# Kernel tuning notes

Measured on AMD Instinct MI355X. Metric: run time of the kernel, lower is better.

## Reference

```python
import jax, jax.numpy as jnp
import numpy as np

B, S, D, H = 2, 2048, 1024, 16
HEAD_DIM = D // H
THETA = 10000.0


def setup_inputs() -> dict:
    key = jax.random.key(0)
    kx, kq, kk, kv, ko = jax.random.split(key, 5)
    w_scale = jnp.float32(D ** -0.5)  # keep logits O(1)
    return {
        "x": jax.random.normal(kx, (B, S, D), dtype=jnp.float32),
        "WQ": jax.random.normal(kq, (D, D), dtype=jnp.float32) * w_scale,
        "WK": jax.random.normal(kk, (D, D), dtype=jnp.float32) * w_scale,
        "WV": jax.random.normal(kv, (D, D), dtype=jnp.float32) * w_scale,
        "WO": jax.random.normal(ko, (D, D), dtype=jnp.float32) * w_scale,
        "token_positions": jnp.arange(S, dtype=jnp.int32),
    }


def _rope(x, pos, theta):
    # x: [B, H, S, dh]; pos: [S]. Interleaved (even, odd) pair rotation.
    dh = x.shape[-1]
    inv_freq = theta ** (-jnp.arange(0, dh, 2, dtype=jnp.float32) / dh)  # [dh/2]
    ang = pos.astype(jnp.float32)[:, None] * inv_freq                    # [S, dh/2]
    cos, sin = jnp.cos(ang), jnp.sin(ang)
    x1, x2 = x[..., 0::2], x[..., 1::2]
    r1 = x1 * cos - x2 * sin
    r2 = x1 * sin + x2 * cos
    return jnp.stack([r1, r2], axis=-1).reshape(x.shape)


def reference(x, WQ, WK, WV, WO, token_positions):
    Bs, Ss, Dm = x.shape
    dh = Dm // H
    # QKV projections (Linear with no bias, y = x @ W.T), split heads -> [B,H,S,dh]
    q = (x @ WQ.T).reshape(Bs, Ss, H, dh).transpose(0, 2, 1, 3)
    k = (x @ WK.T).reshape(Bs, Ss, H, dh).transpose(0, 2, 1, 3)
    v = (x @ WV.T).reshape(Bs, Ss, H, dh).transpose(0, 2, 1, 3)
    q = _rope(q, token_positions, THETA)
    k = _rope(k, token_positions, THETA)
    scores = jnp.einsum("bhqd,bhkd->bhqk", q, k) * jnp.float32(dh ** -0.5)
    causal = jnp.tril(jnp.ones((Ss, Ss), dtype=bool))
    scores = jnp.where(causal, scores, jnp.finfo(scores.dtype).min)
    attn = jax.nn.softmax(scores, axis=-1)
    out = jnp.einsum("bhqk,bhkd->bhqd", attn, v)
    out = out.transpose(0, 2, 1, 3).reshape(Bs, Ss, Dm)
    return out @ WO.T
```

## Files before the change

kernel.cpp:

```cpp
#include <hip/hip_runtime.h>
#include <hip/hip_bf16.h>


#define S_LEN 2048
#define NHEADS 16
#define NEG_SENT -30000.0f

typedef __attribute__((ext_vector_type(8))) short short8;
typedef __attribute__((ext_vector_type(4))) float f32x4;
typedef unsigned int u32;
typedef unsigned short u16;

static __device__ __forceinline__ float bf2f(u16 u) {
  union { u32 i; float f; } v; v.i = ((u32)u) << 16; return v.f;
}
static __device__ __forceinline__ u16 f2bf(float f) {
  union { float f; u32 i; } v; v.f = f;
  u32 u = v.i;
  u32 r = (u + 0x7fffu + ((u >> 16) & 1u)) >> 16;
  return (u16)r;
}
static __device__ __forceinline__ u32 cvtpk(float a, float b) {
  u32 r;
  asm("v_cvt_pk_bf16_f32 %0, %1, %2" : "=v"(r) : "v"(a), "v"(b));
  return r;
}

static __device__ __forceinline__ void glds16(const void* g, void* l) {
  __builtin_amdgcn_global_load_lds((const __attribute__((address_space(1))) u32*)g,
                                   (__attribute__((address_space(3))) u32*)l, 16, 0, 0);
}

__global__ void convert_kernel(const float* __restrict__ x, const float* __restrict__ wq,
                               const float* __restrict__ wk, const float* __restrict__ wv,
                               const float* __restrict__ wo, u16* __restrict__ xb,
                               u16* __restrict__ wb) {
  int i = blockIdx.x * blockDim.x + threadIdx.x;
  const float* src; u16* dst; int off;
  if (i < 1048576) { src = x; dst = xb; off = i; }
  else {
    int j = i - 1048576;
    int widx = j >> 18;
    off = j & 262143;
    src = (widx == 0) ? wq : (widx == 1) ? wk : (widx == 2) ? wv : wo;
    dst = wb + (size_t)widx * 1048576;
  }
  float4 v = ((const float4*)src)[off];
  ushort4 o;
  o.x = f2bf(v.x); o.y = f2bf(v.y); o.z = f2bf(v.z); o.w = f2bf(v.w);
  ((ushort4*)dst)[off] = o;
}

__global__ void rope_kernel(u32* __restrict__ Qb, u32* __restrict__ Kb,
                            const int* __restrict__ pos) {
  int i = blockIdx.x * blockDim.x + threadIdx.x;
  int c = i & 511;
  int rowi = i >> 9;
  int s = rowi & (S_LEN - 1);
  int ip = c & 31;
  float p = (float)pos[s];
  float ang = p * __builtin_exp2f((float)ip * -0.41524101186f);
  float sn, cs;
  sincosf(ang, &sn, &cs);
  u32 v = Qb[i];
  float x1 = bf2f((u16)(v & 0xffff)), x2 = bf2f((u16)(v >> 16));
  float r1 = x1 * cs - x2 * sn, r2 = x1 * sn + x2 * cs;
  Qb[i] = (u32)f2bf(r1) | ((u32)f2bf(r2) << 16);
  v = Kb[i];
  x1 = bf2f((u16)(v & 0xffff)); x2 = bf2f((u16)(v >> 16));
  r1 = x1 * cs - x2 * sn; r2 = x1 * sn + x2 * cs;
  Kb[i] = (u32)f2bf(r1) | ((u32)f2bf(r2) << 16);
}

__global__ void vtrans_kernel(const u16* __restrict__ V, u16* __restrict__ Vt) {
  __shared__ u16 T[64][72];
  const int i = blockIdx.x;
  const int st = i & 31;
  const int bh = i >> 5;
  const int tid = threadIdx.x;
  const int r = tid >> 3, c8 = tid & 7;
  const int s0 = st << 6;
  const int b = bh >> 4, h = bh & 15;
  const u16* src = V + (((size_t)(b * S_LEN + s0 + r)) << 10) + (h << 6) + (c8 << 3);
  uint4 v0 = *(const uint4*)src;
  uint4 v1 = *(const uint4*)(src + (32 << 10));
  *(uint4*)&T[r][c8 << 3] = v0;
  *(uint4*)&T[r + 32][c8 << 3] = v1;
  __syncthreads();
#pragma unroll
  for (int hf = 0; hf < 2; hf++) {
    int d = r + (hf << 5);
    ushort4 o1, o2;
    int sl = c8 << 3;
    o1.x = T[sl + 0][d]; o1.y = T[sl + 1][d]; o1.z = T[sl + 2][d]; o1.w = T[sl + 3][d];
    o2.x = T[sl + 4][d]; o2.y = T[sl + 5][d]; o2.z = T[sl + 6][d]; o2.w = T[sl + 7][d];
    u16* dst = Vt + (((size_t)((bh << 6) + d)) << 11) + s0 + sl;
    *(ushort4*)dst = o1;
    *(ushort4*)(dst + 4) = o2;
  }
}

template <int OUTMODE>
__global__ __launch_bounds__(256, 2) void gemm_bt(const u16* __restrict__ A,
                                                  const u16* __restrict__ B,
                                                  u16* __restrict__ o0, u16* __restrict__ o1,
                                                  u16* __restrict__ o2, float* __restrict__ oF,
                                                  int K) {
  __shared__ u16 As[128 * 64];
  __shared__ u16 Bs[128 * 64];
  const int tid = threadIdx.x, w = tid >> 6, l = tid & 63, l15 = l & 15, l4 = l >> 4;
  const int wr = w >> 1, wc = w & 1;
  const int m0 = blockIdx.y << 7, n0 = blockIdx.x << 7;
  const int r = tid >> 3;
  const int swcol = ((tid & 7) << 4) ^ ((r & 7) << 4);
  const char* Ag = (const char*)A + (((size_t)(m0 + r) * K) << 1) + swcol;
  const char* Bg = (const char*)B + (((size_t)(n0 + r) * K) << 1) + swcol;
  char* AsW = (char*)As + (w << 10);
  char* BsW = (char*)Bs + (w << 10);
  const size_t rowskip = ((size_t)32 * K) << 1;
  f32x4 acc[4][4] = {};
  for (int k0 = 0; k0 < K; k0 += 64) {
    __syncthreads();
    const size_t kb = (size_t)k0 << 1;
#pragma unroll
    for (int i = 0; i < 4; i++) {
      glds16(Ag + kb + (size_t)i * rowskip, AsW + i * 4096);
      glds16(Bg + kb + (size_t)i * rowskip, BsW + i * 4096);
    }
    __syncthreads();
#pragma unroll
    for (int kk = 0; kk < 2; kk++) {
      short8 a[4], b[4];
#pragma unroll
      for (int m = 0; m < 4; m++) {
        int row = (wr << 6) + (m << 4) + l15;
        a[m] = *(const short8*)((const char*)As + row * 128 +
                                (((kk << 6) + (l4 << 4)) ^ ((row & 7) << 4)));
      }
#pragma unroll
      for (int n = 0; n < 4; n++) {
        int row = (wc << 6) + (n << 4) + l15;
        b[n] = *(const short8*)((const char*)Bs + row * 128 +
                                (((kk << 6) + (l4 << 4)) ^ ((row & 7) << 4)));
      }
#pragma unroll
      for (int m = 0; m < 4; m++)
#pragma unroll
        for (int n = 0; n < 4; n++)
          acc[m][n] = __builtin_amdgcn_mfma_f32_16x16x32_bf16(a[m], b[n], acc[m][n], 0, 0, 0);
    }
  }
#pragma unroll
  for (int m = 0; m < 4; m++) {
    int grow_b = m0 + (wr << 6) + (m << 4) + (l4 << 2);
#pragma unroll
    for (int n = 0; n < 4; n++) {
      int gcol = n0 + (wc << 6) + (n << 4) + l15;
#pragma unroll
      for (int j = 0; j < 4; j++) {
        int grow = grow_b + j;
        float v = acc[m][n][j];
        if (OUTMODE == 0) {
          u16* base = (gcol < 1024) ? o0 : ((gcol < 2048) ? o1 : o2);
          base[((size_t)grow << 10) + (gcol & 1023)] = f2bf(v);
        } else {
          oF[((size_t)grow << 10) + gcol] = v;
        }
      }
    }
  }
}

__global__ __launch_bounds__(512, 1) void attn_kernel(const u16* __restrict__ Q,
                                                      const u16* __restrict__ K,
                                                      const u16* __restrict__ Vt,
                                                      u16* __restrict__ O) {
  extern __shared__ __align__(16) char smem[];
  const int tid = threadIdx.x, w = tid >> 6, l = tid & 63, l15 = l & 15, g = l >> 4;
  const int grp = w >> 2, w4 = w & 3;
  const int i = blockIdx.x;
  const int xcd = i & 7, slot = i >> 3;
  const int bh = ((slot >> 3) << 3) | xcd;
  const int p = slot & 7;
  const int b = bh >> 4, h = bh & 15;
  const float C2 = 0.125f * 1.44269504089f;
  const int swz = (l15 & 7) << 4;

  const int gt = tid & 255;
  const int r = gt >> 3;
  const int swc = ((gt & 7) << 4) ^ ((r & 7) << 4);
  const char* Kg = (const char*)K + ((size_t)(b * S_LEN + r) << 11) + (h << 7) + swc;
  const char* Vg = (const char*)Vt + ((size_t)((bh << 6) + r) << 12) + swc;
  char* const KsG = smem + (grp << 15);
  char* const VsG = smem + (grp << 15) + 16384;
  char* const Pw = smem + 65536 + (w << 11);
  float* const oMrg = (float*)smem;
  float* const mlMrg = (float*)(smem + 65536);

#define STAGE(T, BSEL)                                              \
  do {                                                              \
    char* kd = KsG + ((BSEL) << 13) + (w4 << 10);                   \
    char* vd = VsG + ((BSEL) << 13) + (w4 << 10);                   \
    const char* ks = Kg + ((size_t)(T) << 17);                      \
    const char* vs = Vg + ((T) << 7);                               \
    glds16(ks, kd);                                                 \
    glds16(ks + (32 << 11), kd + 4096);                             \
    glds16(vs, vd);                                                 \
    glds16(vs + ((size_t)32 << 12), vd + 4096);                     \
  } while (0)

  auto run_qt = [&](int qt) {
    const int q0 = qt << 7;
    const int nr = qt + 1;

    short8 aQ[2][2];
    {
      const int qrow0 = q0 + (w4 << 5) + l15;
      const u16* qp = Q + (((size_t)(b * S_LEN + qrow0)) << 10) + (h << 6) + (g << 3);
      aQ[0][0] = *(const short8*)qp;
      aQ[0][1] = *(const short8*)(qp + 32);
      aQ[1][0] = *(const short8*)(qp + (16 << 10));
      aQ[1][1] = *(const short8*)(qp + (16 << 10) + 32);
    }
    f32x4 o[2][4] = {};
    float m_r[2] = {NEG_SENT, NEG_SENT}, l_r[2] = {0.f, 0.f};

    STAGE(grp, 0);
    __syncthreads();

    for (int rr = 0; rr < nr; ++rr) {
      const int bsel = rr & 1;
      if (rr + 1 < nr) STAGE(2 * (rr + 1) + grp, bsel ^ 1);
      const char* Kbuf = KsG + (bsel << 13);
      const char* Vbuf = VsG + (bsel << 13);
      const int t = 2 * rr + grp;
      const bool domask = (rr == nr - 1);

      f32x4 s[2][4] = {};
#pragma unroll
      for (int kk = 0; kk < 2; ++kk) {
        short8 aK[4];
#pragma unroll
        for (int n = 0; n < 4; ++n) {
          int row = (n << 4) + l15;
          aK[n] = *(const short8*)(Kbuf + row * 128 + (((kk << 6) + (g << 4)) ^ swz));
        }
        __builtin_amdgcn_s_setprio(1);
#pragma unroll
        for (int n = 0; n < 4; ++n) {
          s[0][n] = __builtin_amdgcn_mfma_f32_16x16x32_bf16(aK[n], aQ[0][kk], s[0][n], 0, 0, 0);
          s[1][n] = __builtin_amdgcn_mfma_f32_16x16x32_bf16(aK[n], aQ[1][kk], s[1][n], 0, 0, 0);
        }
        __builtin_amdgcn_s_setprio(0);
      }
      if (domask) {
#pragma unroll
        for (int qs = 0; qs < 2; ++qs) {
          int qg = q0 + (w4 << 5) + (qs << 4) + l15;
#pragma unroll
          for (int n = 0; n < 4; ++n)
#pragma unroll
            for (int jj = 0; jj < 4; ++jj) {
              int key = (t << 6) + (n << 4) + (g << 2) + jj;
              if (key > qg) s[qs][n][jj] = NEG_SENT;
            }
        }
      }
      float mx2[2];
#pragma unroll
      for (int qs = 0; qs < 2; ++qs) {
        float mx = s[qs][0][0];
#pragma unroll
        for (int n = 0; n < 4; ++n)
#pragma unroll
          for (int jj = 0; jj < 4; ++jj) mx = fmaxf(mx, s[qs][n][jj]);
        mx = fmaxf(mx, __shfl_xor(mx, 16));
        mx = fmaxf(mx, __shfl_xor(mx, 32));
        mx2[qs] = mx;
      }
      if (!__all((mx2[0] - m_r[0] <= 44.f) & (mx2[1] - m_r[1] <= 44.f))) {
        float fac[2];
#pragma unroll
        for (int qs = 0; qs < 2; ++qs) {
          float mn = fmaxf(m_r[qs], mx2[qs]);
          float fc = __builtin_exp2f((m_r[qs] - mn) * C2);
          m_r[qs] = mn;
          l_r[qs] *= fc;
          fac[qs] = fc;
        }
#pragma unroll
        for (int qs = 0; qs < 2; ++qs)
#pragma unroll
          for (int jj = 0; jj < 4; ++jj) {
            float fo = __shfl(fac[qs], (g << 2) + jj, 16);
#pragma unroll
            for (int nd = 0; nd < 4; ++nd) o[qs][nd][jj] *= fo;
          }
      }
      short8 aP[2][2];
#pragma unroll
      for (int qs = 0; qs < 2; ++qs) {
        float mC = m_r[qs] * C2;
        float rs = 0.f;
        u32 pk[8];
#pragma unroll
        for (int n = 0; n < 4; ++n) {
          float p0 = __builtin_exp2f(s[qs][n][0] * C2 - mC);
          float p1 = __builtin_exp2f(s[qs][n][1] * C2 - mC);
          float p2 = __builtin_exp2f(s[qs][n][2] * C2 - mC);
          float p3 = __builtin_exp2f(s[qs][n][3] * C2 - mC);
          rs += (p0 + p1) + (p2 + p3);
          pk[2 * n] = cvtpk(p0, p1);
          pk[2 * n + 1] = cvtpk(p2, p3);
        }
        rs += __shfl_xor(rs, 16);
        rs += __shfl_xor(rs, 32);
        l_r[qs] += rs;
        char* pr = Pw + l15 * 128;
#pragma unroll
        for (int n = 0; n < 4; ++n) {
          uint2 pv;
          pv.x = pk[2 * n];
          pv.y = pk[2 * n + 1];
          *(uint2*)(pr + (((n << 5) + (g << 3)) ^ swz)) = pv;
        }
#pragma unroll
        for (int kk = 0; kk < 2; ++kk)
          aP[qs][kk] = *(const short8*)(Pw + l15 * 128 + ((((kk << 6) + (g << 4))) ^ swz));
      }
#pragma unroll
      for (int kk = 0; kk < 2; ++kk) {
        int co = (kk << 6) + (g << 4);
        __builtin_amdgcn_s_setprio(1);
#pragma unroll
        for (int nd = 0; nd < 4; ++nd) {
          int row = (nd << 4) + l15;
          short8 bV = *(const short8*)(Vbuf + row * 128 + (co ^ swz));
          o[0][nd] = __builtin_amdgcn_mfma_f32_16x16x32_bf16(aP[0][kk], bV, o[0][nd], 0, 0, 0);
          o[1][nd] = __builtin_amdgcn_mfma_f32_16x16x32_bf16(aP[1][kk], bV, o[1][nd], 0, 0, 0);
        }
        __builtin_amdgcn_s_setprio(0);
      }
      __syncthreads();
    }

    if (grp == 1) {
      float* ob = oMrg + (w4 << 11);
#pragma unroll
      for (int qs = 0; qs < 2; ++qs)
#pragma unroll
        for (int nd = 0; nd < 4; ++nd)
          *(f32x4*)(ob + (((qs << 2) | nd) << 8) + (l << 2)) = o[qs][nd];
      float* mb = mlMrg + (w4 << 8);
      mb[l] = m_r[0];
      mb[64 + l] = m_r[1];
      mb[128 + l] = l_r[0];
      mb[192 + l] = l_r[1];
    }
    __syncthreads();
    if (grp == 0) {
      float* ob = oMrg + (w4 << 11);
      float* mb = mlMrg + (w4 << 8);
#pragma unroll
      for (int qs = 0; qs < 2; ++qs) {
        float mB = mb[(qs << 6) + l];
        float lB = mb[128 + (qs << 6) + l];
        float mS = fmaxf(m_r[qs], mB);
        float fA = __builtin_exp2f((m_r[qs] - mS) * C2);
        float fB = __builtin_exp2f((mB - mS) * C2);
        float linv = 1.f / (l_r[qs] * fA + lB * fB);
        float sA = fA * linv, sB = fB * linv;
        f32x4 oB[4];
#pragma unroll
        for (int nd = 0; nd < 4; ++nd)
          oB[nd] = *(const f32x4*)(ob + (((qs << 2) | nd) << 8) + (l << 2));
#pragma unroll
        for (int jj = 0; jj < 4; ++jj) {
          float sAo = __shfl(sA, (g << 2) + jj, 16);
          float sBo = __shfl(sB, (g << 2) + jj, 16);
          int qg = q0 + (w4 << 5) + (qs << 4) + (g << 2) + jj;
          u16* orow = O + (((size_t)(b * S_LEN + qg)) << 10) + (h << 6) + l15;
#pragma unroll
          for (int nd = 0; nd < 4; ++nd)
            orow[nd << 4] = f2bf(o[qs][nd][jj] * sAo + oB[nd][jj] * sBo);
        }
      }
    }
    __syncthreads();
  };

  run_qt(p);
  run_qt(15 - p);
#undef STAGE
}

extern "C" void kernel_launch(void* const* d_in, const int* in_sizes, int n_in,
                              void* d_out, int out_size, void* d_ws, size_t ws_size,
                              hipStream_t stream) {
  (void)in_sizes; (void)n_in; (void)out_size; (void)ws_size;
  const float* x = (const float*)d_in[0];
  const float* wq = (const float*)d_in[1];
  const float* wk = (const float*)d_in[2];
  const float* wv = (const float*)d_in[3];
  const float* wo = (const float*)d_in[4];
  const int* pos = (const int*)d_in[5];
  char* ws = (char*)d_ws;
  u16* xb = (u16*)ws;
  u16* wb = (u16*)(ws + ((size_t)8 << 20));
  u16* Qb = (u16*)(ws + ((size_t)16 << 20));
  u16* Kb = (u16*)(ws + ((size_t)24 << 20));
  u16* Vb = (u16*)(ws + ((size_t)32 << 20));
  u16* Ab = (u16*)(ws + ((size_t)40 << 20));
  u16* Vtg = xb;
  float* out = (float*)d_out;

  convert_kernel<<<8192, 256, 0, stream>>>(x, wq, wk, wv, wo, xb, wb);
  dim3 g1(24, 32);
  gemm_bt<0><<<g1, 256, 0, stream>>>(xb, wb, Qb, Kb, Vb, nullptr, 1024);
  rope_kernel<<<8192, 256, 0, stream>>>((u32*)Qb, (u32*)Kb, pos);
  vtrans_kernel<<<1024, 256, 0, stream>>>(Vb, Vtg);
  attn_kernel<<<256, 512, 81920, stream>>>(Qb, Kb, Vtg, Ab);
  dim3 g3(8, 32);
  gemm_bt<1><<<g3, 256, 0, stream>>>(Ab, wb + (size_t)3 * 1048576, nullptr, nullptr, nullptr, out, 1024);
}
```

Baseline: 118.7 us.

## Fuse RoPE and V transpose into QKV GEMM epilogue

Removes the separate rope and V-transpose kernels. RoPE is now applied inside the QKV GEMM epilogue, using a lane shuffle to fetch each value's pair partner, and V is written straight into transposed layout with 4-element vector stores. This saves two kernel launches and several full read/write passes over Q, K and V. In exchange the epilogue does sincos per output element and writes V in a strided pattern.

```diff
diff --git a/kernel.cpp b/kernel.cpp
--- a/kernel.cpp
+++ b/kernel.cpp
@@ -51,61 +51,12 @@
   ((ushort4*)dst)[off] = o;
 }
 
-__global__ void rope_kernel(u32* __restrict__ Qb, u32* __restrict__ Kb,
-                            const int* __restrict__ pos) {
-  int i = blockIdx.x * blockDim.x + threadIdx.x;
-  int c = i & 511;
-  int rowi = i >> 9;
-  int s = rowi & (S_LEN - 1);
-  int ip = c & 31;
-  float p = (float)pos[s];
-  float ang = p * __builtin_exp2f((float)ip * -0.41524101186f);
-  float sn, cs;
-  sincosf(ang, &sn, &cs);
-  u32 v = Qb[i];
-  float x1 = bf2f((u16)(v & 0xffff)), x2 = bf2f((u16)(v >> 16));
-  float r1 = x1 * cs - x2 * sn, r2 = x1 * sn + x2 * cs;
-  Qb[i] = (u32)f2bf(r1) | ((u32)f2bf(r2) << 16);
-  v = Kb[i];
-  x1 = bf2f((u16)(v & 0xffff)); x2 = bf2f((u16)(v >> 16));
-  r1 = x1 * cs - x2 * sn; r2 = x1 * sn + x2 * cs;
-  Kb[i] = (u32)f2bf(r1) | ((u32)f2bf(r2) << 16);
-}
-
-__global__ void vtrans_kernel(const u16* __restrict__ V, u16* __restrict__ Vt) {
-  __shared__ u16 T[64][72];
-  const int i = blockIdx.x;
-  const int st = i & 31;
-  const int bh = i >> 5;
-  const int tid = threadIdx.x;
-  const int r = tid >> 3, c8 = tid & 7;
-  const int s0 = st << 6;
-  const int b = bh >> 4, h = bh & 15;
-  const u16* src = V + (((size_t)(b * S_LEN + s0 + r)) << 10) + (h << 6) + (c8 << 3);
-  uint4 v0 = *(const uint4*)src;
-  uint4 v1 = *(const uint4*)(src + (32 << 10));
-  *(uint4*)&T[r][c8 << 3] = v0;
-  *(uint4*)&T[r + 32][c8 << 3] = v1;
-  __syncthreads();
-#pragma unroll
-  for (int hf = 0; hf < 2; hf++) {
-    int d = r + (hf << 5);
-    ushort4 o1, o2;
-    int sl = c8 << 3;
-    o1.x = T[sl + 0][d]; o1.y = T[sl + 1][d]; o1.z = T[sl + 2][d]; o1.w = T[sl + 3][d];
-    o2.x = T[sl + 4][d]; o2.y = T[sl + 5][d]; o2.z = T[sl + 6][d]; o2.w = T[sl + 7][d];
-    u16* dst = Vt + (((size_t)((bh << 6) + d)) << 11) + s0 + sl;
-    *(ushort4*)dst = o1;
-    *(ushort4*)(dst + 4) = o2;
-  }
-}
-
 template <int OUTMODE>
 __global__ __launch_bounds__(256, 2) void gemm_bt(const u16* __restrict__ A,
                                                   const u16* __restrict__ B,
                                                   u16* __restrict__ o0, u16* __restrict__ o1,
                                                   u16* __restrict__ o2, float* __restrict__ oF,
-                                                  int K) {
+                                                  const int* __restrict__ pos, int K) {
   __shared__ u16 As[128 * 64];
   __shared__ u16 Bs[128 * 64];
   const int tid = threadIdx.x, w = tid >> 6, l = tid & 63, l15 = l & 15, l4 = l >> 4;
@@ -156,16 +107,36 @@
 #pragma unroll
     for (int n = 0; n < 4; n++) {
       int gcol = n0 + (wc << 6) + (n << 4) + l15;
-#pragma unroll
-      for (int j = 0; j < 4; j++) {
-        int grow = grow_b + j;
-        float v = acc[m][n][j];
-        if (OUTMODE == 0) {
-          u16* base = (gcol < 1024) ? o0 : ((gcol < 2048) ? o1 : o2);
-          base[((size_t)grow << 10) + (gcol & 1023)] = f2bf(v);
-        } else {
-          oF[((size_t)grow << 10) + gcol] = v;
-        }
+      if (OUTMODE == 1) {
+#pragma unroll
+        for (int j = 0; j < 4; j++)
+          oF[((size_t)(grow_b + j) << 10) + gcol] = acc[m][n][j];
+      } else if (gcol < 2048) {
+        u16* base = (gcol < 1024) ? o0 : o1;
+        const int col = gcol & 1023;
+        const int d = col & 63;
+        const float sgn = (d & 1) ? 1.f : -1.f;
+        const float invf = __builtin_exp2f((float)(d >> 1) * -0.41524101186f);
+#pragma unroll
+        for (int j = 0; j < 4; j++) {
+          int grow = grow_b + j;
+          float v = acc[m][n][j];
+          float pv = __shfl_xor(v, 1, 64);
+          float ang = (float)pos[grow & (S_LEN - 1)] * invf;
+          float sn, cs;
+          sincosf(ang, &sn, &cs);
+          base[((size_t)grow << 10) + col] = f2bf(v * cs + pv * sn * sgn);
+        }
+      } else {
+        const int col = gcol & 1023;
+        const int row = (((grow_b >> 11) << 4 | (col >> 6)) << 6) | (col & 63);
+        const int s0 = grow_b & (S_LEN - 1);
+        ushort4 ov;
+        ov.x = f2bf(acc[m][n][0]);
+        ov.y = f2bf(acc[m][n][1]);
+        ov.z = f2bf(acc[m][n][2]);
+        ov.w = f2bf(acc[m][n][3]);
+        *(ushort4*)(o2 + ((size_t)row << 11) + s0) = ov;
       }
     }
   }
@@ -409,17 +380,15 @@
   u16* wb = (u16*)(ws + ((size_t)8 << 20));
   u16* Qb = (u16*)(ws + ((size_t)16 << 20));
   u16* Kb = (u16*)(ws + ((size_t)24 << 20));
-  u16* Vb = (u16*)(ws + ((size_t)32 << 20));
+  u16* Vtg = (u16*)(ws + ((size_t)32 << 20));
   u16* Ab = (u16*)(ws + ((size_t)40 << 20));
-  u16* Vtg = xb;
   float* out = (float*)d_out;
 
   convert_kernel<<<8192, 256, 0, stream>>>(x, wq, wk, wv, wo, xb, wb);
   dim3 g1(24, 32);
-  gemm_bt<0><<<g1, 256, 0, stream>>>(xb, wb, Qb, Kb, Vb, nullptr, 1024);
-  rope_kernel<<<8192, 256, 0, stream>>>((u32*)Qb, (u32*)Kb, pos);
-  vtrans_kernel<<<1024, 256, 0, stream>>>(Vb, Vtg);
+  gemm_bt<0><<<g1, 256, 0, stream>>>(xb, wb, Qb, Kb, Vtg, nullptr, pos, 1024);
   attn_kernel<<<256, 512, 81920, stream>>>(Qb, Kb, Vtg, Ab);
   dim3 g3(8, 32);
-  gemm_bt<1><<<g3, 256, 0, stream>>>(Ab, wb + (size_t)3 * 1048576, nullptr, nullptr, nullptr, out, 1024);
-}
+  gemm_bt<1><<<g3, 256, 0, stream>>>(Ab, wb + (size_t)3 * 1048576, nullptr, nullptr, nullptr,
+                                     out, pos, 1024);
+}
```

Result: slower. 382.3 us (+222.1%).
